# Performance work log

Measured on AMD Instinct MI355X. Metric: run time of the kernel, lower is better.

The kernel has to match this reference:

```python
import jax, jax.numpy as jnp
import numpy as np

NEG = -1e6  # mask fill value used by d2l-style masked_softmax


def setup_inputs() -> dict:
    key = jax.random.key(0)
    kq, kk, kv, kl = jax.random.split(key, 4)
    B, Lq, Lk, D = 8, 2048, 2048, 64
    Q = jax.random.normal(kq, (B, Lq, D), dtype=jnp.float32)
    K = jax.random.normal(kk, (B, Lk, D), dtype=jnp.float32)
    V = jax.random.normal(kv, (B, Lk, D), dtype=jnp.float32)
    valid_len = jax.random.randint(kl, (B,), 1, Lk + 1, dtype=jnp.int64)
    return {"Q": Q, "K": K, "V": V, "valid_len": valid_len}


def reference(Q, K, V, valid_len):
    d = Q.shape[-1]
    scale = 1.0 / jnp.sqrt(jnp.asarray(d, dtype=Q.dtype))
    # scores: [B, Lq, Lk]
    S = jnp.einsum('bqd,bkd->bqk', Q, K) * scale
    Lk = K.shape[1]
    # per-batch key-length mask: position j valid iff j < valid_len[b]
    mask = jnp.arange(Lk)[None, None, :] < valid_len[:, None, None]
    S = jnp.where(mask, S, NEG)
    A = jax.nn.softmax(S, axis=-1)
    return jnp.einsum('bqk,bkd->bqd', A, V)
```

## Files before the change

kernel.cpp:

```cpp
#include <hip/hip_runtime.h>
#include <hip/hip_bf16.h>


constexpr int B_  = 8;
constexpr int L_  = 2048;
constexpr int D_  = 64;
constexpr int BQ  = 128;
constexpr int BK  = 64;
constexpr int LDK = 72;
constexpr int NQ  = L_ / BQ;

constexpr float QSCALE = 0.125f * 1.44269504088896340736f;

using bf16x8 = __attribute__((ext_vector_type(8))) __bf16;
using f32x4  = __attribute__((ext_vector_type(4))) float;

union frag_u { unsigned u[4]; bf16x8 v; };

#if __has_builtin(__builtin_amdgcn_exp2f)
#define EXP2(x) __builtin_amdgcn_exp2f(x)
#else
#define EXP2(x) exp2f(x)
#endif

__device__ __forceinline__ unsigned pack2(float lo, float hi) {
    __hip_bfloat162 h = __float22bfloat162_rn(make_float2(lo, hi));
    return *(unsigned*)&h;
}
__device__ __forceinline__ int sniff_valid(const int* vl, int b) {
    const int p1 = vl[1];
    return (p1 == 0) ? vl[2 * b] : vl[b];
}

__global__ __launch_bounds__(256, 2) void attn_fwd(
    const float* __restrict__ Q, const float* __restrict__ K,
    const float* __restrict__ V, const int* __restrict__ vl,
    float* __restrict__ O, float* __restrict__ Opart,
    float* __restrict__ lpart, int nsplit, int splitk)
{
    __shared__ __align__(16) unsigned short Ks[2][BK * LDK];
    __shared__ __align__(16) unsigned short Vt[2][D_ * LDK];
    __shared__ __align__(16) unsigned short Ps[4 * 32 * LDK];

    const int id   = blockIdx.x;
    const int qt   = id & (NQ - 1);
    const int b    = (id >> 4) & (B_ - 1);
    const int s    = id >> 7;
    const int tid  = threadIdx.x;
    const int wave = tid >> 6;
    const int lan  = tid & 15;
    const int quad = (tid >> 4) & 3;

    const int valid  = sniff_valid(vl, b);
    const int kstart = s * splitk;
    if (kstart >= valid) return;
    const int kend   = min(kstart + splitk, valid);
    const int ntiles = (kend - kstart + BK - 1) / BK;

    const float* Kg = K + (size_t)b * L_ * D_;
    const float* Vg = V + (size_t)b * L_ * D_;

    const int krow = tid >> 4, kc0 = (tid & 15) * 4;
    const int vk0  = (tid & 31) * 2, vd0 = (tid >> 5) * 8;

    float4 kr[4], vr[4];
    {
        const float* ks = Kg + (size_t)(kstart + krow) * D_ + kc0;
        #pragma unroll
        for (int p = 0; p < 4; ++p) kr[p] = *(const float4*)(ks + (size_t)p * 16 * D_);
        const float* vs = Vg + (size_t)(kstart + vk0) * D_ + vd0;
        vr[0] = *(const float4*)(vs);
        vr[1] = *(const float4*)(vs + 4);
        vr[2] = *(const float4*)(vs + D_);
        vr[3] = *(const float4*)(vs + D_ + 4);
    }

    bf16x8 aq[2][2];
    #pragma unroll
    for (int g = 0; g < 2; ++g) {
        const float* qs = Q + ((size_t)b * L_ + qt * BQ + wave * 32 + g * 16 + lan) * D_;
        float4 q0 = *(const float4*)(qs + quad * 8);
        float4 q1 = *(const float4*)(qs + quad * 8 + 4);
        float4 q2 = *(const float4*)(qs + 32 + quad * 8);
        float4 q3 = *(const float4*)(qs + 32 + quad * 8 + 4);
        frag_u f0, f1;
        f0.u[0] = pack2(q0.x * QSCALE, q0.y * QSCALE);
        f0.u[1] = pack2(q0.z * QSCALE, q0.w * QSCALE);
        f0.u[2] = pack2(q1.x * QSCALE, q1.y * QSCALE);
        f0.u[3] = pack2(q1.z * QSCALE, q1.w * QSCALE);
        f1.u[0] = pack2(q2.x * QSCALE, q2.y * QSCALE);
        f1.u[1] = pack2(q2.z * QSCALE, q2.w * QSCALE);
        f1.u[2] = pack2(q3.x * QSCALE, q3.y * QSCALE);
        f1.u[3] = pack2(q3.z * QSCALE, q3.w * QSCALE);
        aq[g][0] = f0.v;
        aq[g][1] = f1.v;
    }

    f32x4 oacc[2][4];
    #pragma unroll
    for (int g = 0; g < 2; ++g)
        #pragma unroll
        for (int c = 0; c < 4; ++c) oacc[g][c] = (f32x4){0.f, 0.f, 0.f, 0.f};
    float lsum[2] = {0.f, 0.f};

    unsigned short* Pw = &Ps[wave * 32 * LDK];

    int cur = 0;
    for (int t = 0; t < ntiles; ++t) {
        const int kt = kstart + t * BK;
        unsigned short* Kb = &Ks[cur][0];
        unsigned short* Vb = &Vt[cur][0];

        #pragma unroll
        for (int p = 0; p < 4; ++p) {
            uint2 w = make_uint2(pack2(kr[p].x, kr[p].y), pack2(kr[p].z, kr[p].w));
            *(uint2*)&Kb[(p * 16 + krow) * LDK + kc0] = w;
        }
        {
            const float* a = (const float*)&vr[0];
            const float* c = (const float*)&vr[2];
            #pragma unroll
            for (int j = 0; j < 8; ++j)
                *(unsigned*)&Vb[(vd0 + j) * LDK + vk0] = pack2(a[j], c[j]);
        }
        __syncthreads();

        if (t + 1 < ntiles) {
            const int kn = kt + BK;
            const float* ks = Kg + (size_t)(kn + krow) * D_ + kc0;
            #pragma unroll
            for (int p = 0; p < 4; ++p) kr[p] = *(const float4*)(ks + (size_t)p * 16 * D_);
            const float* vs = Vg + (size_t)(kn + vk0) * D_ + vd0;
            vr[0] = *(const float4*)(vs);
            vr[1] = *(const float4*)(vs + 4);
            vr[2] = *(const float4*)(vs + D_);
            vr[3] = *(const float4*)(vs + D_ + 4);
        }
        asm volatile("" ::: "memory");

        #pragma unroll
        for (int c = 0; c < 4; ++c) {
            bf16x8 ak0 = *(const bf16x8*)&Kb[(c*16 + lan) * LDK + quad * 8];
            bf16x8 ak1 = *(const bf16x8*)&Kb[(c*16 + lan) * LDK + 32 + quad * 8];
            f32x4 z0 = (f32x4){0.f, 0.f, 0.f, 0.f};
            f32x4 z1 = (f32x4){0.f, 0.f, 0.f, 0.f};
            z0 = __builtin_amdgcn_mfma_f32_16x16x32_bf16(ak0, aq[0][0], z0, 0, 0, 0);
            z1 = __builtin_amdgcn_mfma_f32_16x16x32_bf16(ak0, aq[1][0], z1, 0, 0, 0);
            z0 = __builtin_amdgcn_mfma_f32_16x16x32_bf16(ak1, aq[0][1], z0, 0, 0, 0);
            z1 = __builtin_amdgcn_mfma_f32_16x16x32_bf16(ak1, aq[1][1], z1, 0, 0, 0);

            const int kbase = kt + c * 16 + quad * 4;
            float p0[4], p1[4];
            #pragma unroll
            for (int r = 0; r < 4; ++r) {
                const bool ok = (kbase + r) < valid;
                p0[r] = ok ? EXP2(z0[r]) : 0.f;
                p1[r] = ok ? EXP2(z1[r]) : 0.f;
                lsum[0] += p0[r];
                lsum[1] += p1[r];
            }
            *(uint2*)&Pw[lan * LDK + c * 16 + quad * 4] =
                make_uint2(pack2(p0[0], p0[1]), pack2(p0[2], p0[3]));
            *(uint2*)&Pw[(16 + lan) * LDK + c * 16 + quad * 4] =
                make_uint2(pack2(p1[0], p1[1]), pack2(p1[2], p1[3]));
        }

        bf16x8 ap[2][2];
        #pragma unroll
        for (int g = 0; g < 2; ++g) {
            ap[g][0] = *(const bf16x8*)&Pw[(g*16 + lan) * LDK + quad * 8];
            ap[g][1] = *(const bf16x8*)&Pw[(g*16 + lan) * LDK + 32 + quad * 8];
        }
        #pragma unroll
        for (int c = 0; c < 4; ++c) {
            bf16x8 bv0 = *(const bf16x8*)&Vb[(c*16 + lan) * LDK + quad * 8];
            bf16x8 bv1 = *(const bf16x8*)&Vb[(c*16 + lan) * LDK + 32 + quad * 8];
            #pragma unroll
            for (int g = 0; g < 2; ++g) {
                oacc[g][c] = __builtin_amdgcn_mfma_f32_16x16x32_bf16(ap[g][0], bv0, oacc[g][c], 0, 0, 0);
                oacc[g][c] = __builtin_amdgcn_mfma_f32_16x16x32_bf16(ap[g][1], bv1, oacc[g][c], 0, 0, 0);
            }
        }
        cur ^= 1;
    }

    #pragma unroll
    for (int g = 0; g < 2; ++g) {
        lsum[g] += __shfl_xor(lsum[g], 16);
        lsum[g] += __shfl_xor(lsum[g], 32);
    }

    const int rowbase = qt * BQ + wave * 32;
    if (nsplit == 1) {
        #pragma unroll
        for (int g = 0; g < 2; ++g) {
            float inv[4];
            #pragma unroll
            for (int r = 0; r < 4; ++r)
                inv[r] = 1.0f / __shfl(lsum[g], quad * 4 + r);
            float* Og = O + ((size_t)b * L_ + rowbase + g * 16) * D_;
            #pragma unroll
            for (int c = 0; c < 4; ++c)
                #pragma unroll
                for (int r = 0; r < 4; ++r)
                    Og[(size_t)(quad * 4 + r) * D_ + c * 16 + lan] = oacc[g][c][r] * inv[r];
        }
    } else {
        #pragma unroll
        for (int g = 0; g < 2; ++g) {
            float* Og = Opart + ((size_t)s * B_ * L_ + (size_t)b * L_ + rowbase + g * 16) * D_;
            #pragma unroll
            for (int c = 0; c < 4; ++c)
                #pragma unroll
                for (int r = 0; r < 4; ++r)
                    Og[(size_t)(quad * 4 + r) * D_ + c * 16 + lan] = oacc[g][c][r];
            if (quad == 0)
                lpart[(size_t)s * B_ * L_ + (size_t)b * L_ + rowbase + g * 16 + lan] = lsum[g];
        }
    }
}

__global__ __launch_bounds__(256) void attn_combine(
    const float* __restrict__ Opart, const float* __restrict__ lpart,
    const int* __restrict__ vl, float* __restrict__ O,
    int nsplit, int splitk)
{
    const int idx = blockIdx.x * 256 + threadIdx.x;
    const int row = idx >> 4;
    const int b   = row >> 11;
    const int off = (idx & 15) * 4;
    const int valid = sniff_valid(vl, b);
    const int ns = min(nsplit, (valid + splitk - 1) / splitk);

    float Lsum = 0.f;
    float4 acc = make_float4(0.f, 0.f, 0.f, 0.f);
    for (int s = 0; s < ns; ++s) {
        Lsum += lpart[s * (B_ * L_) + row];
        float4 o4 = *(const float4*)&Opart[(size_t)s * (B_ * L_ * D_) + (size_t)row * D_ + off];
        acc.x += o4.x; acc.y += o4.y; acc.z += o4.z; acc.w += o4.w;
    }
    const float inv = 1.0f / Lsum;
    acc.x *= inv; acc.y *= inv; acc.z *= inv; acc.w *= inv;
    *(float4*)&O[(size_t)row * D_ + off] = acc;
}

extern "C" void kernel_launch(void* const* d_in, const int* in_sizes, int n_in,
                              void* d_out, int out_size, void* d_ws, size_t ws_size,
                              hipStream_t stream) {
    const float* Q  = (const float*)d_in[0];
    const float* K  = (const float*)d_in[1];
    const float* V  = (const float*)d_in[2];
    const int*   vl = (const int*)d_in[3];
    float* O = (float*)d_out;

    auto need = [](int n) {
        return (size_t)n * (B_ * L_ * D_ + B_ * L_) * sizeof(float);
    };
    int nsplit = 1;
    if      (ws_size >= need(4)) nsplit = 4;
    else if (ws_size >= need(2)) nsplit = 2;
    const int splitk = L_ / nsplit;

    float* Opart = (float*)d_ws;
    float* lpart = Opart + (size_t)nsplit * B_ * L_ * D_;

    attn_fwd<<<dim3(nsplit * B_ * NQ), 256, 0, stream>>>(
        Q, K, V, vl, O, Opart, lpart, nsplit, splitk);
    if (nsplit > 1)
        attn_combine<<<dim3((B_ * L_ * D_ / 4) / 256), 256, 0, stream>>>(
            Opart, lpart, vl, O, nsplit, splitk);
}
```

Measured before the change: 88.16 us.

## Split key range adaptively per batch into balanced halves, cap split at two

```diff
diff --git a/kernel.cpp b/kernel.cpp
--- a/kernel.cpp
+++ b/kernel.cpp
@@ -36,7 +36,7 @@
     const float* __restrict__ Q, const float* __restrict__ K,
     const float* __restrict__ V, const int* __restrict__ vl,
     float* __restrict__ O, float* __restrict__ Opart,
-    float* __restrict__ lpart, int nsplit, int splitk)
+    float* __restrict__ lpart, int maxsplit)
 {
     __shared__ __align__(16) unsigned short Ks[2][BK * LDK];
     __shared__ __align__(16) unsigned short Vt[2][D_ * LDK];
@@ -52,10 +52,12 @@
     const int quad = (tid >> 4) & 3;
 
     const int valid  = sniff_valid(vl, b);
-    const int kstart = s * splitk;
-    if (kstart >= valid) return;
-    const int kend   = min(kstart + splitk, valid);
-    const int ntiles = (kend - kstart + BK - 1) / BK;
+    const int vtiles = (valid + BK - 1) >> 6;
+    const int ns = (maxsplit == 2 && vtiles > 16) ? 2 : 1;
+    if (s >= ns) return;
+    const int half   = (vtiles + 1) >> 1;
+    const int kstart = (s == 0) ? 0 : half * BK;
+    const int ntiles = (ns == 1) ? vtiles : ((s == 0) ? half : vtiles - half);
 
     const float* Kg = K + (size_t)b * L_ * D_;
     const float* Vg = V + (size_t)b * L_ * D_;
@@ -191,7 +193,7 @@
     }
 
     const int rowbase = qt * BQ + wave * 32;
-    if (nsplit == 1) {
+    if (ns == 1) {
         #pragma unroll
         for (int g = 0; g < 2; ++g) {
             float inv[4];
@@ -222,25 +224,25 @@
 
 __global__ __launch_bounds__(256) void attn_combine(
     const float* __restrict__ Opart, const float* __restrict__ lpart,
-    const int* __restrict__ vl, float* __restrict__ O,
-    int nsplit, int splitk)
+    const int* __restrict__ vl, float* __restrict__ O)
 {
     const int idx = blockIdx.x * 256 + threadIdx.x;
     const int row = idx >> 4;
     const int b   = row >> 11;
     const int off = (idx & 15) * 4;
-    const int valid = sniff_valid(vl, b);
-    const int ns = min(nsplit, (valid + splitk - 1) / splitk);
-
-    float Lsum = 0.f;
-    float4 acc = make_float4(0.f, 0.f, 0.f, 0.f);
-    for (int s = 0; s < ns; ++s) {
-        Lsum += lpart[s * (B_ * L_) + row];
-        float4 o4 = *(const float4*)&Opart[(size_t)s * (B_ * L_ * D_) + (size_t)row * D_ + off];
-        acc.x += o4.x; acc.y += o4.y; acc.z += o4.z; acc.w += o4.w;
-    }
+    const int valid  = sniff_valid(vl, b);
+    const int vtiles = (valid + BK - 1) >> 6;
+    if (vtiles <= 16) return;
+
+    const float Lsum = lpart[row] + lpart[B_ * L_ + row];
+    float4 a0 = *(const float4*)&Opart[(size_t)row * D_ + off];
+    float4 a1 = *(const float4*)&Opart[(size_t)(B_ * L_ * D_) + (size_t)row * D_ + off];
     const float inv = 1.0f / Lsum;
-    acc.x *= inv; acc.y *= inv; acc.z *= inv; acc.w *= inv;
+    float4 acc;
+    acc.x = (a0.x + a1.x) * inv;
+    acc.y = (a0.y + a1.y) * inv;
+    acc.z = (a0.z + a1.z) * inv;
+    acc.w = (a0.w + a1.w) * inv;
     *(float4*)&O[(size_t)row * D_ + off] = acc;
 }
 
@@ -253,20 +255,15 @@
     const int*   vl = (const int*)d_in[3];
     float* O = (float*)d_out;
 
-    auto need = [](int n) {
-        return (size_t)n * (B_ * L_ * D_ + B_ * L_) * sizeof(float);
-    };
-    int nsplit = 1;
-    if      (ws_size >= need(4)) nsplit = 4;
-    else if (ws_size >= need(2)) nsplit = 2;
-    const int splitk = L_ / nsplit;
+    const size_t need2 = (size_t)2 * (B_ * L_ * D_ + B_ * L_) * sizeof(float);
+    const int maxsplit = (ws_size >= need2) ? 2 : 1;
 
     float* Opart = (float*)d_ws;
-    float* lpart = Opart + (size_t)nsplit * B_ * L_ * D_;
-
-    attn_fwd<<<dim3(nsplit * B_ * NQ), 256, 0, stream>>>(
-        Q, K, V, vl, O, Opart, lpart, nsplit, splitk);
-    if (nsplit > 1)
+    float* lpart = Opart + (size_t)2 * B_ * L_ * D_;
+
+    attn_fwd<<<dim3(maxsplit * B_ * NQ), 256, 0, stream>>>(
+        Q, K, V, vl, O, Opart, lpart, maxsplit);
+    if (maxsplit == 2)
         attn_combine<<<dim3((B_ * L_ * D_ / 4) / 256), 256, 0, stream>>>(
-            Opart, lpart, vl, O, nsplit, splitk);
-}
+            Opart, lpart, vl, O);
+}
```

Result: no change. 88.86 us (+0.8%).
